# Performance work log

Measured on AMD Instinct MI355X. Metric: run time of the kernel, lower is better.

## Reference

```python
import jax, jax.numpy as jnp
import numpy as np

B, S, H = 2, 2048, 2048
NH, NKV, HD = 16, 4, 128
THETA = 10000.0


def _rope_cos_sin(seq_len, head_dim, theta, dtype):
    inv_freq = 1.0 / (theta ** (jnp.arange(0, head_dim, 2, dtype=jnp.float32) / head_dim))
    t = jnp.arange(seq_len, dtype=jnp.float32)
    freqs = t[:, None] * inv_freq[None, :]          # [S, HD/2]
    emb = jnp.concatenate([freqs, freqs], axis=-1)  # [S, HD]
    return jnp.cos(emb).astype(dtype), jnp.sin(emb).astype(dtype)


def _rotate_half(x):
    d = x.shape[-1] // 2
    return jnp.concatenate([-x[..., d:], x[..., :d]], axis=-1)


def setup_inputs() -> dict:
    key = jax.random.key(0)
    ks = jax.random.split(key, 5)
    x = jax.random.normal(ks[0], (B, S, H), dtype=jnp.float32)
    Wq = jax.random.normal(ks[1], (NH * HD, H), dtype=jnp.float32) * 0.02
    Wk = jax.random.normal(ks[2], (NKV * HD, H), dtype=jnp.float32) * 0.02
    Wv = jax.random.normal(ks[3], (NKV * HD, H), dtype=jnp.float32) * 0.02
    Wo = jax.random.normal(ks[4], (H, H), dtype=jnp.float32) * 0.02
    causal = jnp.tril(jnp.ones((S, S), dtype=bool))
    attention_mask = jnp.where(causal, 0.0, -1e9).astype(jnp.float32)[None, None]  # [1,1,S,S]
    return {"x": x, "attention_mask": attention_mask, "Wq": Wq, "Wk": Wk, "Wv": Wv, "Wo": Wo}


def reference(x, attention_mask, Wq, Wk, Wv, Wo):
    b, s, _ = x.shape
    q = (x @ Wq.T).reshape(b, s, NH, HD).transpose(0, 2, 1, 3)    # [b,nh,s,hd]
    k = (x @ Wk.T).reshape(b, s, NKV, HD).transpose(0, 2, 1, 3)   # [b,nkv,s,hd]
    v = (x @ Wv.T).reshape(b, s, NKV, HD).transpose(0, 2, 1, 3)
    cos, sin = _rope_cos_sin(s, HD, THETA, x.dtype)               # [s,hd] each
    cos = cos[None, None]; sin = sin[None, None]
    q = q * cos + _rotate_half(q) * sin
    k = k * cos + _rotate_half(k) * sin
    rep = NH // NKV
    k = jnp.repeat(k, rep, axis=1)                                 # [b,nh,s,hd]
    v = jnp.repeat(v, rep, axis=1)
    scores = jnp.einsum('bhqd,bhkd->bhqk', q, k) / jnp.sqrt(jnp.asarray(HD, x.dtype))
    scores = scores + attention_mask
    attn = jax.nn.softmax(scores, axis=-1)
    out = jnp.einsum('bhqk,bhkd->bhqd', attn, v)                   # [b,nh,s,hd]
    out = out.transpose(0, 2, 1, 3).reshape(b, s, NH * HD)
    return out @ Wo.T
```

## Files before the change

### kernel.cpp

```cpp
#include <hip/hip_runtime.h>

typedef unsigned short u16;
typedef __bf16 bf16x8 __attribute__((ext_vector_type(8)));
typedef float f32x4 __attribute__((ext_vector_type(4)));
typedef short s16x4 __attribute__((ext_vector_type(4)));

#define S_LEN  2048
#define NHEADS 16
#define NKVH   4
#define HDIM   128
#define BB     2
#define MROWS  4096
#define QKV_N  3072
#define HID    2048

__device__ __forceinline__ u16 f2b(float f) {
  union { float f; unsigned u; } x; x.f = f;
  unsigned r = x.u + 0x7fffu + ((x.u >> 16) & 1u);
  return (u16)(r >> 16);
}
__device__ __forceinline__ float b2f(u16 v) {
  union { unsigned u; float f; } x; x.u = ((unsigned)v) << 16;
  return x.f;
}
__device__ __forceinline__ void gload_lds16(const u16* g, u16* l) {
  __builtin_amdgcn_global_load_lds((__attribute__((address_space(1))) void*)g,
                                   (__attribute__((address_space(3))) void*)l,
                                   16, 0, 0);
}
__device__ __forceinline__ unsigned cvtpk(float lo, float hi) {
  unsigned r;
  asm("v_cvt_pk_bf16_f32 %0, %1, %2" : "=v"(r) : "v"(lo), "v"(hi));
  return r;
}
__device__ __forceinline__ float fexp2(float x) {
  float r;
  asm("v_exp_f32 %0, %1" : "=v"(r) : "v"(x));
  return r;
}
#if __has_builtin(__builtin_amdgcn_mfma_f32_16x16x16bf16_1k)
__device__ __forceinline__ f32x4 mfma16(s16x4 a, s16x4 b, f32x4 c) {
  return __builtin_amdgcn_mfma_f32_16x16x16bf16_1k(a, b, c, 0, 0, 0);
}
#else
__device__ __forceinline__ f32x4 mfma16(s16x4 a, s16x4 b, f32x4 c) {
  asm("v_mfma_f32_16x16x16_bf16 %0, %1, %2, %0" : "+v"(c) : "v"(a), "v"(b));
  return c;
}
#endif

#define SBAR() do { __builtin_amdgcn_sched_barrier(0); \
                    __builtin_amdgcn_s_barrier();      \
                    __builtin_amdgcn_sched_barrier(0); } while (0)

#define PB_X   8192
#define PB_WQ  (PB_X + 4096)
#define PB_WK  (PB_WQ + 1024)
#define PB_WV  (PB_WK + 1024)
#define PB_WO  (PB_WV + 4096)
#define PB_CS  (PB_WO + 512)
__global__ void k_prep(const float* __restrict__ x,
                       const float* __restrict__ Wq, const float* __restrict__ Wk,
                       const float* __restrict__ Wv, const float* __restrict__ Wo,
                       u16* __restrict__ xb, u16* __restrict__ Wqkvb,
                       u16* __restrict__ Wob, float* __restrict__ cs)
{
  const int bid = blockIdx.x, tid = threadIdx.x;
  const float* src; u16* dst; int i;
  if (bid < PB_X)       { i = bid * 256 + tid;            src = x;  dst = xb; }
  else if (bid < PB_WQ) { i = (bid - PB_X) * 256 + tid;   src = Wq; dst = Wqkvb; }
  else if (bid < PB_WK) { i = (bid - PB_WQ) * 256 + tid;  src = Wk; dst = Wqkvb + (size_t)2048 * HID; }
  else if (bid < PB_WV) { i = (bid - PB_WK) * 256 + tid;  src = Wv; dst = Wqkvb + (size_t)2560 * HID; }
  else if (bid < PB_WO) { i = (bid - PB_WV) * 256 + tid;  src = Wo; dst = Wob; }
  else {
    const int p = (bid - PB_WO) * 256 + tid;
    const int s = p >> 6, j = p & 63;
    float inv = expf(-(float)j * 0.14391156831212787f);
    float ang = (float)s * inv;
    float c, sn; sincosf(ang, &sn, &c);
    cs[p * 2 + 0] = c; cs[p * 2 + 1] = sn;
    return;
  }
  float4 v = ((const float4*)src)[i];
  ushort4 o;
  o.x = f2b(v.x); o.y = f2b(v.y); o.z = f2b(v.z); o.w = f2b(v.w);
  ((ushort4*)dst)[i] = o;
}

#define MFMA_GRP(AV, BV, MO, NO)                                              \
  __builtin_amdgcn_s_setprio(1);                                              \
  _Pragma("unroll") for (int kk = 0; kk < 2; ++kk)                            \
  _Pragma("unroll") for (int mm = 0; mm < 4; ++mm)                            \
  _Pragma("unroll") for (int nn = 0; nn < 2; ++nn)                            \
    acc[(MO) + mm][(NO) + nn] = __builtin_amdgcn_mfma_f32_16x16x32_bf16(      \
        AV[kk][mm], BV[kk][nn], acc[(MO) + mm][(NO) + nn], 0, 0, 0);          \
  __builtin_amdgcn_s_setprio(0);

template <int OUT_BF16>
__global__ __launch_bounds__(512, 2) void k_gemm256(
    const u16* __restrict__ A, const u16* __restrict__ Bm, void* __restrict__ Cv,
    int M, int N, int K)
{
  __shared__ u16 AL[2][2][8192];
  __shared__ u16 BL[2][2][8192];
  const int tid = threadIdx.x;
  const int wave = tid >> 6, lane = tid & 63;
  const int l15 = lane & 15, l4 = lane >> 4;
  const int wr = wave >> 2, wc = wave & 3;
  const int gx = gridDim.x;
  const int nwg = gx * gridDim.y;
  int bid = blockIdx.y * gx + blockIdx.x;
  bid = (bid & 7) * (nwg >> 3) + (bid >> 3);
  const int col0 = (bid % gx) * 256, row0 = (bid / gx) * 256;

  int srcOff[2], dstD[2];
#pragma unroll
  for (int li = 0; li < 2; ++li) {
    const int D = (li * 512 + tid) * 16;
    const int off_p = D & 1023, si = D >> 10;
    const int off_l = off_p ^ (((off_p >> 9) & 1) << 5);
    const int R = si >> 1, C = si & 1;
    const int row = R * 16 + (off_l >> 6);
    const int colb = C * 64 + (off_l & 63);
    srcOff[li] = row * K + (colb >> 1);
    dstD[li] = D;
  }
  const int laneoff = (l15 * 64 + l4 * 16) ^ ((l15 >> 3) << 5);

  auto stage = [&](const u16* __restrict__ G, int grow0, int kb, u16* lds) {
#pragma unroll
    for (int li = 0; li < 2; ++li)
      gload_lds16(G + (size_t)grow0 * K + kb + srcOff[li],
                  (u16*)((char*)lds + dstD[li]));
  };

  f32x4 acc[8][4];
#pragma unroll
  for (int m = 0; m < 8; ++m)
#pragma unroll
    for (int n = 0; n < 4; ++n) acc[m][n] = f32x4{0.f, 0.f, 0.f, 0.f};

  const int nk = K >> 6;
  stage(A,  row0,       0,  &AL[0][0][0]);
  stage(A,  row0 + 128, 0,  &AL[0][1][0]);
  stage(Bm, col0,       0,  &BL[0][0][0]);
  stage(Bm, col0 + 128, 0,  &BL[0][1][0]);
  stage(A,  row0,       64, &AL[1][0][0]);
  stage(A,  row0 + 128, 64, &AL[1][1][0]);
  asm volatile("s_waitcnt vmcnt(4)" ::: "memory");
  SBAR();

  for (int t = 0; t < nk; ++t) {
    const int bi = t & 1;
    const bool sB = (t + 1 < nk);
    const bool sA = (t + 2 < nk);
    const char* Ab = (const char*)&AL[bi][wr][0];
    const char* Bb = (const char*)&BL[bi][wc >> 1][0] + (wc & 1) * 8192;
    bf16x8 a0[2][4], a1[2][4], b0[2][2], b1[2][2];
#pragma unroll
    for (int kk = 0; kk < 2; ++kk)
#pragma unroll
      for (int m = 0; m < 4; ++m)
        a0[kk][m] = *(const bf16x8*)(Ab + m * 2048 + kk * 1024 + laneoff);
#pragma unroll
    for (int kk = 0; kk < 2; ++kk)
#pragma unroll
      for (int n = 0; n < 2; ++n)
        b0[kk][n] = *(const bf16x8*)(Bb + n * 2048 + kk * 1024 + laneoff);
    if (sB) stage(Bm, col0, (t + 1) * 64, &BL[bi ^ 1][0][0]);
    SBAR();
    MFMA_GRP(a0, b0, 0, 0);
    SBAR();
#pragma unroll
    for (int kk = 0; kk < 2; ++kk)
#pragma unroll
      for (int m = 0; m < 4; ++m)
        a1[kk][m] = *(const bf16x8*)(Ab + (m + 4) * 2048 + kk * 1024 + laneoff);
    if (sB) stage(Bm, col0 + 128, (t + 1) * 64, &BL[bi ^ 1][1][0]);
    SBAR();
    MFMA_GRP(a1, b0, 4, 0);
    SBAR();
#pragma unroll
    for (int kk = 0; kk < 2; ++kk)
#pragma unroll
      for (int n = 0; n < 2; ++n)
        b1[kk][n] = *(const bf16x8*)(Bb + (n + 2) * 2048 + kk * 1024 + laneoff);
    if (sA) stage(A, row0, (t + 2) * 64, &AL[bi][0][0]);
    SBAR();
    MFMA_GRP(a1, b1, 4, 2);
    SBAR();
    if (sA) {
      stage(A, row0 + 128, (t + 2) * 64, &AL[bi][1][0]);
      asm volatile("s_waitcnt vmcnt(4)" ::: "memory");
    } else if (sB) {
      asm volatile("s_waitcnt vmcnt(0)" ::: "memory");
    }
    SBAR();
    MFMA_GRP(a0, b1, 0, 2);
    SBAR();
  }

#pragma unroll
  for (int m = 0; m < 8; ++m) {
    const int r = row0 + wr * 128 + m * 16 + l4 * 4;
#pragma unroll
    for (int n = 0; n < 4; ++n) {
      const int c = col0 + wc * 64 + n * 16 + l15;
#pragma unroll
      for (int j = 0; j < 4; ++j) {
        const float v = acc[m][n][j];
        if (OUT_BF16) ((u16*)Cv)[(size_t)(r + j) * N + c] = f2b(v);
        else          ((float*)Cv)[(size_t)(r + j) * N + c] = v;
      }
    }
  }
}

template <int OUT_BF16>
__global__ __launch_bounds__(256) void k_gemm_bt(
    const u16* __restrict__ A, const u16* __restrict__ Bm, void* __restrict__ Cv,
    int M, int N, int K)
{
  __shared__ u16 Al[2][128 * 32];
  __shared__ u16 Bl[2][128 * 32];
  const int tid = threadIdx.x;
  const int wave = tid >> 6, lane = tid & 63;
  const int l15 = lane & 15, l4 = lane >> 4;
  const int wr = wave >> 1, wc = wave & 1;
  const int row0 = blockIdx.y * 128, col0 = blockIdx.x * 128;

  f32x4 zero = {0.f, 0.f, 0.f, 0.f};
  f32x4 acc[4][4];
#pragma unroll
  for (int m = 0; m < 4; ++m)
#pragma unroll
    for (int n = 0; n < 4; ++n) acc[m][n] = zero;

  const int e0 = lane * 8;
  auto stage = [&](int buf, int kb) {
#pragma unroll
    for (int it = 0; it < 2; ++it) {
      const int chunk = it * 4 + wave;
      const int e = chunk * 512 + e0;
      const int r = e >> 5, c = e & 31;
      gload_lds16(A + (size_t)(row0 + r) * K + kb + c, &Al[buf][chunk * 512]);
      gload_lds16(Bm + (size_t)(col0 + r) * K + kb + c, &Bl[buf][chunk * 512]);
    }
  };

  stage(0, 0);
  asm volatile("s_waitcnt vmcnt(0)" ::: "memory");
  SBAR();
  int cur = 0;
  for (int kb = 0; kb < K; kb += 32) {
    if (kb + 32 < K) stage(cur ^ 1, kb + 32);
    bf16x8 af[4], bfv[4];
#pragma unroll
    for (int m = 0; m < 4; ++m)
      af[m] = *(const bf16x8*)(&Al[cur][(wr * 64 + m * 16 + l15) * 32 + l4 * 8]);
#pragma unroll
    for (int n = 0; n < 4; ++n)
      bfv[n] = *(const bf16x8*)(&Bl[cur][(wc * 64 + n * 16 + l15) * 32 + l4 * 8]);
    __builtin_amdgcn_s_setprio(1);
#pragma unroll
    for (int m = 0; m < 4; ++m)
#pragma unroll
      for (int n = 0; n < 4; ++n)
        acc[m][n] = __builtin_amdgcn_mfma_f32_16x16x32_bf16(af[m], bfv[n], acc[m][n], 0, 0, 0);
    __builtin_amdgcn_s_setprio(0);
    asm volatile("s_waitcnt vmcnt(0)" ::: "memory");
    SBAR();
    cur ^= 1;
  }
#pragma unroll
  for (int m = 0; m < 4; ++m) {
    const int r = row0 + wr * 64 + m * 16 + l4 * 4;
#pragma unroll
    for (int n = 0; n < 4; ++n) {
      const int c = col0 + wc * 64 + n * 16 + l15;
#pragma unroll
      for (int j = 0; j < 4; ++j) {
        const float v = acc[m][n][j];
        if (OUT_BF16) ((u16*)Cv)[(size_t)(r + j) * N + c] = f2b(v);
        else          ((float*)Cv)[(size_t)(r + j) * N + c] = v;
      }
    }
  }
}

__global__ __launch_bounds__(256) void k_ropev(
    const u16* __restrict__ qkv, const float* __restrict__ cs,
    u16* __restrict__ Qr, u16* __restrict__ Kr, u16* __restrict__ Vt)
{
  const int blk = blockIdx.x;
  const int b = blk >> 8, s0 = (blk & 255) << 3;
  const int tid = threadIdx.x;
  const float S2 = 0.08838834764831845f * 1.4426950408889634f;
#pragma unroll
  for (int p = tid; p < 8192; p += 256) {
    const int s = p >> 10, rem = p & 1023, h = rem >> 6, j = rem & 63;
    const int sg = s0 + s;
    const float c = cs[(sg * 64 + j) * 2], sn = cs[(sg * 64 + j) * 2 + 1];
    const u16* src = qkv + (size_t)(b * S_LEN + sg) * QKV_N + h * 128;
    const float x0 = b2f(src[j]), x1 = b2f(src[64 + j]);
    const size_t base = ((size_t)(b * NHEADS + h) * S_LEN + sg) * HDIM;
    Qr[base + j]      = f2b((x0 * c - x1 * sn) * S2);
    Qr[base + 64 + j] = f2b((x1 * c + x0 * sn) * S2);
  }
#pragma unroll
  for (int p = tid; p < 2048; p += 256) {
    const int s = p >> 8, rem = p & 255, h = rem >> 6, j = rem & 63;
    const int sg = s0 + s;
    const float c = cs[(sg * 64 + j) * 2], sn = cs[(sg * 64 + j) * 2 + 1];
    const u16* src = qkv + (size_t)(b * S_LEN + sg) * QKV_N + 2048 + h * 128;
    const float x0 = b2f(src[j]), x1 = b2f(src[64 + j]);
    const size_t base = ((size_t)(b * NKVH + h) * S_LEN + sg) * HDIM;
    Kr[base + j]      = f2b(x0 * c - x1 * sn);
    Kr[base + 64 + j] = f2b(x1 * c + x0 * sn);
  }
#pragma unroll
  for (int vi = 0; vi < 2; ++vi) {
    const int idx = vi * 256 + tid, h = idx >> 7, d = idx & 127;
    union { u16 u[8]; uint4 v; } bb;
#pragma unroll
    for (int s = 0; s < 8; ++s)
      bb.u[s] = qkv[(size_t)(b * S_LEN + s0 + s) * QKV_N + 2560 + idx];
    *(uint4*)(Vt + ((size_t)(b * NKVH + h) * HDIM + d) * S_LEN + s0) = bb.v;
  }
}

__global__ __launch_bounds__(256) void k_attn(
    const u16* __restrict__ Q, const u16* __restrict__ Kr,
    const u16* __restrict__ Vt, u16* __restrict__ Out)
{
  __shared__ u16 Kl[2][64 * 128];
  __shared__ u16 Vl[2][128 * 64];
  const int tid = threadIdx.x;
  const int wave = tid >> 6, lane = tid & 63;
  const int l15 = lane & 15, l4 = lane >> 4;
  const int bid = blockIdx.x;
  const int xg = bid & 7;
  const int b = xg >> 2, kvh = xg & 3;
  const int h = kvh * 4 + ((bid >> 3) & 3);
  const int qti = bid >> 5;
  const int qt = (bid < 256) ? qti : 23 - qti;

  const u16* Kg = Kr + (size_t)(b * NKVH + kvh) * S_LEN * HDIM;
  const u16* Vg = Vt + (size_t)(b * NKVH + kvh) * HDIM * S_LEN;

  int ko[4], vo[4];
#pragma unroll
  for (int it = 0; it < 4; ++it) {
    const int c = it * 4 + wave;
    const int L = c * 1024 + lane * 16;
    const int r = L >> 8;  const int w2 = (L & 255) ^ ((r & 7) << 4);
    ko[it] = r * HDIM + (w2 >> 1);
    const int d = L >> 7;  const int wv = (L & 127) ^ ((d & 7) << 4);
    vo[it] = d * S_LEN + (wv >> 1);
  }

  const int qw0 = qt * 128 + wave * 32;
  const u16* Qg = Q + ((size_t)(b * NHEADS + h) * S_LEN + qw0) * HDIM;

  bf16x8 qf[2][4];
#pragma unroll
  for (int mq = 0; mq < 2; ++mq)
#pragma unroll
    for (int kc = 0; kc < 4; ++kc)
      qf[mq][kc] = *(const bf16x8*)(Qg + (mq * 16 + l15) * HDIM + kc * 32 + l4 * 8);

  f32x4 zero = {0.f, 0.f, 0.f, 0.f};
  f32x4 oacc[2][8];
#pragma unroll
  for (int mq = 0; mq < 2; ++mq)
#pragma unroll
    for (int i = 0; i < 8; ++i) oacc[mq][i] = zero;
  float m_r[2] = {-1e30f, -1e30f}, l_p[2] = {0.f, 0.f};

  const int nt = 2 * qt + 2;
  const int qgl = qw0 + l15;
  int cur = 0;

#pragma unroll
  for (int it = 0; it < 4; ++it)
    gload_lds16(Kg + ko[it], &Kl[0][(it * 4 + wave) * 512]);
#pragma unroll
  for (int it = 0; it < 4; ++it)
    gload_lds16(Vg + (size_t)vo[it], &Vl[0][(it * 4 + wave) * 512]);

  for (int t = 0; t < nt; ++t) {
    const int kt = t * 64;
    asm volatile("s_waitcnt vmcnt(0)" ::: "memory");
    SBAR();
    const char* Kb = (const char*)(cur ? &Kl[1][0] : &Kl[0][0]);
    const char* Vb = (const char*)(cur ? &Vl[1][0] : &Vl[0][0]);
    f32x4 s[2][4];
#pragma unroll
    for (int mq = 0; mq < 2; ++mq)
#pragma unroll
      for (int n = 0; n < 4; ++n) s[mq][n] = zero;
    __builtin_amdgcn_s_setprio(1);
#pragma unroll
    for (int n = 0; n < 4; ++n) {
      const int row = n * 16 + l15;
#pragma unroll
      for (int kc = 0; kc < 4; ++kc) {
        const int ab = (row * 256 + kc * 64 + l4 * 16) ^ ((row & 7) << 4);
        bf16x8 kf = *(const bf16x8*)(Kb + ab);
        s[0][n] = __builtin_amdgcn_mfma_f32_16x16x32_bf16(kf, qf[0][kc], s[0][n], 0, 0, 0);
        s[1][n] = __builtin_amdgcn_mfma_f32_16x16x32_bf16(kf, qf[1][kc], s[1][n], 0, 0, 0);
      }
    }
    __builtin_amdgcn_s_setprio(0);
    const int hasNext = (t + 1 < nt);
    if (hasNext) {
      const int ktn = kt + 64;
      u16* Kn = cur ? &Kl[0][0] : &Kl[1][0];
      u16* Vn = cur ? &Vl[0][0] : &Vl[1][0];
#pragma unroll
      for (int it = 0; it < 4; ++it)
        gload_lds16(Kg + (size_t)ktn * HDIM + ko[it], Kn + (it * 4 + wave) * 512);
#pragma unroll
      for (int it = 0; it < 4; ++it)
        gload_lds16(Vg + (size_t)vo[it] + ktn, Vn + (it * 4 + wave) * 512);
    }
    if (kt + 63 > qw0) {
#pragma unroll
      for (int mq = 0; mq < 2; ++mq)
#pragma unroll
        for (int n = 0; n < 4; ++n)
#pragma unroll
          for (int j = 0; j < 4; ++j)
            if (kt + n * 16 + l4 * 4 + j > qgl + mq * 16) s[mq][n][j] = -1e30f;
    }
    float pm[2];
#pragma unroll
    for (int mq = 0; mq < 2; ++mq) {
      pm[mq] = s[mq][0][0];
#pragma unroll
      for (int n = 0; n < 4; ++n)
#pragma unroll
        for (int j = 0; j < 4; ++j) pm[mq] = fmaxf(pm[mq], s[mq][n][j]);
    }
    const bool ok = (pm[0] <= m_r[0] + 11.5416f) && (pm[1] <= m_r[1] + 11.5416f);
    if (!__all(ok)) {
#pragma unroll
      for (int mq = 0; mq < 2; ++mq) {
        float pf = fmaxf(pm[mq], __shfl_xor(pm[mq], 16, 64));
        pf = fmaxf(pf, __shfl_xor(pf, 32, 64));
        const float mn = fmaxf(m_r[mq], pf);
        const float sc = fexp2(m_r[mq] - mn);
        m_r[mq] = mn;
        l_p[mq] *= sc;
        float scq[4];
#pragma unroll
        for (int j = 0; j < 4; ++j) scq[j] = __shfl(sc, l4 * 4 + j, 64);
#pragma unroll
        for (int nd = 0; nd < 8; ++nd)
#pragma unroll
          for (int j = 0; j < 4; ++j) oacc[mq][nd][j] *= scq[j];
      }
    }
    union { unsigned u[2]; s16x4 v; } a[2][4];
#pragma unroll
    for (int mq = 0; mq < 2; ++mq)
#pragma unroll
      for (int n = 0; n < 4; ++n) {
        const float p0 = fexp2(s[mq][n][0] - m_r[mq]);
        const float p1 = fexp2(s[mq][n][1] - m_r[mq]);
        const float p2 = fexp2(s[mq][n][2] - m_r[mq]);
        const float p3 = fexp2(s[mq][n][3] - m_r[mq]);
        l_p[mq] += (p0 + p1) + (p2 + p3);
        a[mq][n].u[0] = cvtpk(p0, p1);
        a[mq][n].u[1] = cvtpk(p2, p3);
      }
    __builtin_amdgcn_s_setprio(1);
#pragma unroll
    for (int n = 0; n < 4; ++n) {
      s16x4 vf[8];
#pragma unroll
      for (int nd = 0; nd < 8; ++nd) {
        const int d = nd * 16 + l15;
        vf[nd] = *(const s16x4*)(Vb + ((d * 128 + n * 32 + l4 * 8) ^ ((d & 7) << 4)));
      }
#pragma unroll
      for (int nd = 0; nd < 8; ++nd) {
        oacc[0][nd] = mfma16(a[0][n].v, vf[nd], oacc[0][nd]);
        oacc[1][nd] = mfma16(a[1][n].v, vf[nd], oacc[1][nd]);
      }
    }
    __builtin_amdgcn_s_setprio(0);
    cur ^= 1;
  }

#pragma unroll
  for (int mq = 0; mq < 2; ++mq) {
    float lp = l_p[mq];
    lp += __shfl_xor(lp, 16, 64);
    lp += __shfl_xor(lp, 32, 64);
    float il[4];
#pragma unroll
    for (int j = 0; j < 4; ++j) il[j] = 1.f / __shfl(lp, l4 * 4 + j, 64);
    const size_t obase =
        ((size_t)b * S_LEN + qw0 + mq * 16 + l4 * 4) * HID + h * HDIM;
#pragma unroll
    for (int nd = 0; nd < 8; ++nd)
#pragma unroll
      for (int j = 0; j < 4; ++j)
        Out[obase + (size_t)j * HID + nd * 16 + l15] = f2b(oacc[mq][nd][j] * il[j]);
  }
}

extern "C" void kernel_launch(void* const* d_in, const int* in_sizes, int n_in,
                              void* d_out, int out_size, void* d_ws, size_t ws_size,
                              hipStream_t stream)
{
  const float* x  = (const float*)d_in[0];
  const float* Wq = (const float*)d_in[2];
  const float* Wk = (const float*)d_in[3];
  const float* Wv = (const float*)d_in[4];
  const float* Wo = (const float*)d_in[5];
  float* out = (float*)d_out;

  u16* xb    = (u16*)d_ws;
  u16* Wqkvb = xb    + (size_t)MROWS * HID;
  u16* Wob   = Wqkvb + (size_t)QKV_N * HID;
  u16* qkv   = Wob   + (size_t)HID * HID;
  u16* Qr    = qkv   + (size_t)MROWS * QKV_N;
  u16* Kr    = Qr    + (size_t)BB * NHEADS * S_LEN * HDIM;
  u16* Vt    = Kr    + (size_t)BB * NKVH * S_LEN * HDIM;
  u16* attn  = Vt    + (size_t)BB * NKVH * S_LEN * HDIM;
  float* cs  = (float*)(attn + (size_t)MROWS * HID);

  k_prep<<<dim3(PB_CS), 256, 0, stream>>>(x, Wq, Wk, Wv, Wo, xb, Wqkvb, Wob, cs);
  k_gemm256<1><<<dim3(QKV_N / 256, MROWS / 256), 512, 0, stream>>>(xb, Wqkvb, qkv, MROWS, QKV_N, HID);
  k_ropev<<<dim3(BB * 256), 256, 0, stream>>>(qkv, cs, Qr, Kr, Vt);
  k_attn<<<dim3(512), 256, 0, stream>>>(Qr, Kr, Vt, attn);
  k_gemm_bt<0><<<dim3(HID / 128, MROWS / 128), 256, 0, stream>>>(attn, Wob, out, MROWS, HID, HID);
}
```

Baseline: 223.0 us.

## Split long causal attention tiles across two blocks with a merge kernel

```diff
diff --git a/kernel.cpp b/kernel.cpp
--- a/kernel.cpp
+++ b/kernel.cpp
@@ -331,7 +331,8 @@
 
 __global__ __launch_bounds__(256) void k_attn(
     const u16* __restrict__ Q, const u16* __restrict__ Kr,
-    const u16* __restrict__ Vt, u16* __restrict__ Out)
+    const u16* __restrict__ Vt, u16* __restrict__ Out,
+    float* __restrict__ Opart, float* __restrict__ Ml)
 {
   __shared__ u16 Kl[2][64 * 128];
   __shared__ u16 Vl[2][128 * 64];
@@ -339,11 +340,24 @@
   const int wave = tid >> 6, lane = tid & 63;
   const int l15 = lane & 15, l4 = lane >> 4;
   const int bid = blockIdx.x;
-  const int xg = bid & 7;
-  const int b = xg >> 2, kvh = xg & 3;
-  const int h = kvh * 4 + ((bid >> 3) & 3);
-  const int qti = bid >> 5;
-  const int qt = (bid < 256) ? qti : 23 - qti;
+  int b, kvh, hsub, qt, t0, t1, item;
+  if (bid < 512) {
+    kvh = bid & 3; b = (bid >> 2) & 1; hsub = (bid >> 3) & 3;
+    const int half = (bid >> 5) & 1;
+    qt = 15 - (bid >> 6);
+    const int mid = qt + 1, ntt = 2 * qt + 2;
+    t0 = half ? mid : 0;
+    t1 = half ? ntt : mid;
+    item = (((b * 16 + kvh * 4 + hsub) << 3) | (qt - 8)) * 2 + half;
+  } else {
+    const int idx = bid - 512;
+    kvh = idx & 3; b = (idx >> 2) & 1; hsub = (idx >> 3) & 3;
+    qt = 7 - (idx >> 5);
+    t0 = 0; t1 = 2 * qt + 2;
+    item = -1;
+  }
+  const int h = kvh * 4 + hsub;
+  const int bh = b * NHEADS + h;
 
   const u16* Kg = Kr + (size_t)(b * NKVH + kvh) * S_LEN * HDIM;
   const u16* Vg = Vt + (size_t)(b * NKVH + kvh) * HDIM * S_LEN;
@@ -360,7 +374,7 @@
   }
 
   const int qw0 = qt * 128 + wave * 32;
-  const u16* Qg = Q + ((size_t)(b * NHEADS + h) * S_LEN + qw0) * HDIM;
+  const u16* Qg = Q + ((size_t)bh * S_LEN + qw0) * HDIM;
 
   bf16x8 qf[2][4];
 #pragma unroll
@@ -377,18 +391,17 @@
     for (int i = 0; i < 8; ++i) oacc[mq][i] = zero;
   float m_r[2] = {-1e30f, -1e30f}, l_p[2] = {0.f, 0.f};
 
-  const int nt = 2 * qt + 2;
   const int qgl = qw0 + l15;
   int cur = 0;
 
 #pragma unroll
   for (int it = 0; it < 4; ++it)
-    gload_lds16(Kg + ko[it], &Kl[0][(it * 4 + wave) * 512]);
+    gload_lds16(Kg + (size_t)(t0 * 64) * HDIM + ko[it], &Kl[0][(it * 4 + wave) * 512]);
 #pragma unroll
   for (int it = 0; it < 4; ++it)
-    gload_lds16(Vg + (size_t)vo[it], &Vl[0][(it * 4 + wave) * 512]);
-
-  for (int t = 0; t < nt; ++t) {
+    gload_lds16(Vg + (size_t)vo[it] + t0 * 64, &Vl[0][(it * 4 + wave) * 512]);
+
+  for (int t = t0; t < t1; ++t) {
     const int kt = t * 64;
     asm volatile("s_waitcnt vmcnt(0)" ::: "memory");
     SBAR();
@@ -412,7 +425,7 @@
       }
     }
     __builtin_amdgcn_s_setprio(0);
-    const int hasNext = (t + 1 < nt);
+    const int hasNext = (t + 1 < t1);
     if (hasNext) {
       const int ktn = kt + 64;
       u16* Kn = cur ? &Kl[0][0] : &Kl[1][0];
@@ -498,16 +511,56 @@
     float lp = l_p[mq];
     lp += __shfl_xor(lp, 16, 64);
     lp += __shfl_xor(lp, 32, 64);
-    float il[4];
-#pragma unroll
-    for (int j = 0; j < 4; ++j) il[j] = 1.f / __shfl(lp, l4 * 4 + j, 64);
-    const size_t obase =
-        ((size_t)b * S_LEN + qw0 + mq * 16 + l4 * 4) * HID + h * HDIM;
-#pragma unroll
-    for (int nd = 0; nd < 8; ++nd)
-#pragma unroll
-      for (int j = 0; j < 4; ++j)
-        Out[obase + (size_t)j * HID + nd * 16 + l15] = f2b(oacc[mq][nd][j] * il[j]);
+    const int rloc = wave * 32 + mq * 16;
+    if (item >= 0) {
+      if (l4 == 0) {
+        Ml[((size_t)item * 2 + 0) * 128 + rloc + l15] = m_r[mq];
+        Ml[((size_t)item * 2 + 1) * 128 + rloc + l15] = lp;
+      }
+#pragma unroll
+      for (int nd = 0; nd < 8; ++nd)
+#pragma unroll
+        for (int j = 0; j < 4; ++j)
+          Opart[((size_t)item * 128 + rloc + l4 * 4 + j) * 128 + nd * 16 + l15] =
+              oacc[mq][nd][j];
+    } else {
+      float il[4];
+#pragma unroll
+      for (int j = 0; j < 4; ++j) il[j] = 1.f / __shfl(lp, l4 * 4 + j, 64);
+      const size_t obase =
+          ((size_t)b * S_LEN + qw0 + mq * 16 + l4 * 4) * HID + h * HDIM;
+#pragma unroll
+      for (int nd = 0; nd < 8; ++nd)
+#pragma unroll
+        for (int j = 0; j < 4; ++j)
+          Out[obase + (size_t)j * HID + nd * 16 + l15] = f2b(oacc[mq][nd][j] * il[j]);
+    }
+  }
+}
+
+__global__ __launch_bounds__(256) void k_merge(
+    const float* __restrict__ Opart, const float* __restrict__ Ml,
+    u16* __restrict__ Out)
+{
+  const int mb = blockIdx.x;
+  const int bh = mb & 31, qidx = mb >> 5;
+  const int b = bh >> 4, h = bh & 15;
+  const int qt = qidx + 8;
+  const int i0 = ((bh << 3) | qidx) * 2, i1 = i0 + 1;
+  const int tid = threadIdx.x;
+  const int col = tid & 127;
+  for (int r = tid >> 7; r < 128; r += 2) {
+    const float m1 = Ml[((size_t)i0 * 2 + 0) * 128 + r];
+    const float l1 = Ml[((size_t)i0 * 2 + 1) * 128 + r];
+    const float m2 = Ml[((size_t)i1 * 2 + 0) * 128 + r];
+    const float l2 = Ml[((size_t)i1 * 2 + 1) * 128 + r];
+    const float m = fmaxf(m1, m2);
+    const float e1 = fexp2(m1 - m), e2 = fexp2(m2 - m);
+    const float il = 1.f / (l1 * e1 + l2 * e2);
+    const float o1 = Opart[((size_t)i0 * 128 + r) * 128 + col];
+    const float o2 = Opart[((size_t)i1 * 128 + r) * 128 + col];
+    Out[((size_t)b * S_LEN + qt * 128 + r) * HID + h * HDIM + col] =
+        f2b((o1 * e1 + o2 * e2) * il);
   }
 }
 
@@ -531,10 +584,13 @@
   u16* Vt    = Kr    + (size_t)BB * NKVH * S_LEN * HDIM;
   u16* attn  = Vt    + (size_t)BB * NKVH * S_LEN * HDIM;
   float* cs  = (float*)(attn + (size_t)MROWS * HID);
+  float* Opart = cs + (size_t)2048 * 128;
+  float* Ml    = Opart + (size_t)512 * 128 * 128;
 
   k_prep<<<dim3(PB_CS), 256, 0, stream>>>(x, Wq, Wk, Wv, Wo, xb, Wqkvb, Wob, cs);
   k_gemm256<1><<<dim3(QKV_N / 256, MROWS / 256), 512, 0, stream>>>(xb, Wqkvb, qkv, MROWS, QKV_N, HID);
   k_ropev<<<dim3(BB * 256), 256, 0, stream>>>(qkv, cs, Qr, Kr, Vt);
-  k_attn<<<dim3(512), 256, 0, stream>>>(Qr, Kr, Vt, attn);
+  k_attn<<<dim3(768), 256, 0, stream>>>(Qr, Kr, Vt, attn, Opart, Ml);
+  k_merge<<<dim3(256), 256, 0, stream>>>(Opart, Ml, attn);
   k_gemm_bt<0><<<dim3(HID / 128, MROWS / 128), 256, 0, stream>>>(attn, Wob, out, MROWS, HID, HID);
 }
```

After: 262.5 us. +17.7%, slower.
